# Performance work log

Measured on AMD Instinct MI355X. Metric: run time of the kernel, lower is better.

The kernel has to match this reference:

```python
import jax, jax.numpy as jnp
import numpy as np

NUM_LAYERS = 4
HID = 512
EMB = 512
VOCAB = 50000
SOU_LEN = 256
TAR_LEN = 50
BATCH = 8
VEXT = VOCAB + SOU_LEN


def _gru_layer(x, h0, wih, whh, bih, bhh):
    # x: [B,T,in], h0: [B,H]; PyTorch GRU gate order: r, z, n
    def step(h, xt):
        gi = xt @ wih.T + bih
        gh = h @ whh.T + bhh
        ir, iz, inn = jnp.split(gi, 3, axis=-1)
        hr, hz, hn = jnp.split(gh, 3, axis=-1)
        r = jax.nn.sigmoid(ir + hr)
        z = jax.nn.sigmoid(iz + hz)
        n = jnp.tanh(inn + r * hn)
        h_new = (1.0 - z) * n + z * h
        return h_new, h_new
    _, ys = jax.lax.scan(step, h0, jnp.swapaxes(x, 0, 1))
    return jnp.swapaxes(ys, 0, 1)


def _forward(sou, tar, hidden, encoder_outputs, extended_length,
             emb, gru_wih, gru_whh, gru_bih, gru_bhh,
             fc_enc_w, fc_enc_b, fc_dec_w, fc_dec_b, v_w,
             fc_out1_w, fc_out1_b, fc_out2_w, fc_out2_b,
             g1_w, g1_b, g2_w, g2_b, g3_w, g3_b):
    emb = emb.at[0].set(0.0)  # padding_idx=0 (also zeroes its grad)
    tar_emb = emb[tar]  # [B,T,E]
    # pack_padded_sequence: only first `length` steps processed, rest padded with 0
    lengths = jnp.maximum(jnp.sum(tar > 0, axis=-1), 1)
    x = tar_emb
    for l in range(gru_wih.shape[0]):
        x = _gru_layer(x, hidden[l], gru_wih[l], gru_whh[l], gru_bih[l], gru_bhh[l])
    t_idx = jnp.arange(x.shape[1])
    dec_out = jnp.where((t_idx[None, :] < lengths[:, None])[:, :, None], x, 0.0)  # [B,T,H]
    # additive (Bahdanau) attention
    e1 = encoder_outputs @ fc_enc_w.T + fc_enc_b          # [B,S,H]
    e2 = dec_out @ fc_dec_w.T + fc_dec_b                  # [B,T,H]
    energy = jnp.tanh(e1[:, None, :, :] + e2[:, :, None, :])  # [B,T,S,H]
    scores = jnp.einsum('btsh,h->bts', energy, v_w)
    scores = jnp.where((sou == 0)[:, None, :], -jnp.inf, scores)
    atten = jax.nn.softmax(scores, axis=-1)               # [B,T,S]
    weighted = jnp.einsum('bts,bsh->bth', atten, encoder_outputs)
    all_out = jnp.concatenate([weighted, dec_out], axis=-1)  # [B,T,2H]
    mid = all_out @ fc_out2_w.T + fc_out2_b
    logits = mid @ fc_out1_w.T + fc_out1_b                # [B,T,VEXT]
    # extended-vocab mask (vectorized version of the per-batch python loop)
    col = jnp.arange(logits.shape[-1])
    valid = col[None, None, :] < (VOCAB + extended_length)[:, None, None]
    logits = jnp.where(valid, logits, -1e9)
    output_gen = jax.nn.softmax(logits, axis=-1)
    # copy mechanism: scatter-add attention into extended vocab (replaces sparse one-hot bmm)
    def _scatter(att_b, sou_b):
        return jnp.zeros((att_b.shape[0], VEXT), att_b.dtype).at[:, sou_b].add(att_b)
    output_copy = jax.vmap(_scatter)(atten, sou)          # [B,T,VEXT]
    gate = jax.nn.sigmoid(
        jnp.einsum('bth,h->bt', weighted, g1_w) + g1_b[0]
        + jnp.einsum('bth,h->bt', dec_out, g2_w) + g2_b[0]
        + jnp.einsum('bte,e->bt', tar_emb, g3_w) + g3_b[0])[:, :, None]
    output = (1.0 - gate) * output_gen + gate * output_copy
    return output, atten


def setup_inputs() -> dict:
    key = jax.random.key(0)
    ks = jax.random.split(key, 24)
    s = 0.02
    return {
        'sou': jax.random.randint(ks[0], (BATCH, SOU_LEN), 0, VEXT),
        'tar': jax.random.randint(ks[1], (BATCH, TAR_LEN), 0, VEXT),
        'hidden': jax.random.normal(ks[2], (NUM_LAYERS, BATCH, HID), jnp.float32),
        'encoder_outputs': jax.random.normal(ks[3], (BATCH, SOU_LEN, HID), jnp.float32),
        'extended_length': jax.random.randint(ks[4], (BATCH,), 0, SOU_LEN),
        'emb': jax.random.normal(ks[5], (VEXT, EMB), jnp.float32) * s,
        'gru_wih': jax.random.normal(ks[6], (NUM_LAYERS, 3 * HID, EMB), jnp.float32) * s,
        'gru_whh': jax.random.normal(ks[7], (NUM_LAYERS, 3 * HID, HID), jnp.float32) * s,
        'gru_bih': jax.random.normal(ks[8], (NUM_LAYERS, 3 * HID), jnp.float32) * s,
        'gru_bhh': jax.random.normal(ks[9], (NUM_LAYERS, 3 * HID), jnp.float32) * s,
        'fc_enc_w': jax.random.normal(ks[10], (HID, HID), jnp.float32) * s,
        'fc_enc_b': jax.random.normal(ks[11], (HID,), jnp.float32) * s,
        'fc_dec_w': jax.random.normal(ks[12], (HID, HID), jnp.float32) * s,
        'fc_dec_b': jax.random.normal(ks[13], (HID,), jnp.float32) * s,
        'v_w': jax.random.normal(ks[14], (HID,), jnp.float32) * s,
        'fc_out1_w': jax.random.normal(ks[15], (VEXT, HID), jnp.float32) * s,
        'fc_out1_b': jax.random.normal(ks[16], (VEXT,), jnp.float32) * s,
        'fc_out2_w': jax.random.normal(ks[17], (HID, 2 * HID), jnp.float32) * s,
        'fc_out2_b': jax.random.normal(ks[18], (HID,), jnp.float32) * s,
        'g1_w': jax.random.normal(ks[19], (HID,), jnp.float32) * s,
        'g1_b': jnp.zeros((1,), jnp.float32),
        'g2_w': jax.random.normal(ks[20], (HID,), jnp.float32) * s,
        'g2_b': jnp.zeros((1,), jnp.float32),
        'g3_w': jax.random.normal(ks[21], (EMB,), jnp.float32) * s,
        'g3_b': jnp.zeros((1,), jnp.float32),
    }


def reference(sou, tar, hidden, encoder_outputs, extended_length,
              emb, gru_wih, gru_whh, gru_bih, gru_bhh,
              fc_enc_w, fc_enc_b, fc_dec_w, fc_dec_b, v_w,
              fc_out1_w, fc_out1_b, fc_out2_w, fc_out2_b,
              g1_w, g1_b, g2_w, g2_b, g3_w, g3_b):
    return _forward(sou, tar, hidden, encoder_outputs, extended_length,
                    emb, gru_wih, gru_whh, gru_bih, gru_bhh,
                    fc_enc_w, fc_enc_b, fc_dec_w, fc_dec_b, v_w,
                    fc_out1_w, fc_out1_b, fc_out2_w, fc_out2_b,
                    g1_w, g1_b, g2_w, g2_b, g3_w, g3_b)
```

## Files before the change

### kernel.cpp

```cpp
#include <hip/hip_runtime.h>

typedef unsigned short u16;
typedef unsigned int u32;
typedef unsigned long long u64;

using bf16x8 = __attribute__((ext_vector_type(8))) short;
using f32x4  = __attribute__((ext_vector_type(4))) float;

#define VOCAB 50000
#define VEXT  50256
#define OUT_AT_OFF 20102400L

__device__ __forceinline__ u16 f2b(float f) {
  u32 x = __float_as_uint(f);
  u32 r = (x + 0x7fffu + ((x >> 16) & 1u)) >> 16;
  return (u16)r;
}

__device__ __forceinline__ u32 sload32(const u32* p) {
  return __hip_atomic_load(p, __ATOMIC_RELAXED, __HIP_MEMORY_SCOPE_SYSTEM);
}
__device__ __forceinline__ u64 sload64(const u64* p) {
  return __hip_atomic_load(p, __ATOMIC_RELAXED, __HIP_MEMORY_SCOPE_SYSTEM);
}
__device__ __forceinline__ void sstore64(u64* p, u64 v) {
  __hip_atomic_store(p, v, __ATOMIC_RELAXED, __HIP_MEMORY_SCOPE_SYSTEM);
}
__device__ __forceinline__ bf16x8 sload8x(const u64* p) {
  union { u64 u[2]; bf16x8 v; } x;
  x.u[0] = sload64(p); x.u[1] = sload64(p + 1);
  return x.v;
}
__device__ __forceinline__ void wait_cnt(const u32* c, u32 target) {
  unsigned it = 0;
  while (sload32(c) < target) {
    __builtin_amdgcn_s_sleep(2);
    if (++it > (1u << 20)) break;
  }
  asm volatile("" ::: "memory");
}

__global__ void k_conv(const float* __restrict__ src, u16* __restrict__ dst,
                       long realN, long totalN) {
  long i = (long)blockIdx.x * 256 + threadIdx.x;
  if (i >= totalN) return;
  float v = (i < realN) ? src[i] : 0.f;
  dst[i] = f2b(v);
}

__global__ void k_h0b(const float* __restrict__ hidden, u16* __restrict__ h0B) {
  int i = blockIdx.x * 256 + threadIdx.x;
  int l = i >> 13, rem = i & 8191, rr = rem >> 9, k = rem & 511;
  float v = (rr < 8) ? hidden[((long)l * 8 + rr) * 512 + k] : 0.f;
  h0B[i] = f2b(v);
}

__global__ __launch_bounds__(256) void k_prep(const int* __restrict__ tar,
                                              const float* __restrict__ emb,
                                              const float* __restrict__ g3w,
                                              u16* __restrict__ xB0,
                                              float* __restrict__ g3dot) {
  int r = blockIdx.x;
  int tid = threadIdx.x;
  int idx = tar[r];
  __shared__ float red[256];
  float p = 0.f;
  for (int k = tid; k < 512; k += 256) {
    float v = (idx == 0) ? 0.f : emb[(long)idx * 512 + k];
    xB0[(long)r * 512 + k] = f2b(v);
    p += v * g3w[k];
  }
  red[tid] = p; __syncthreads();
  for (int o = 128; o > 0; o >>= 1) { if (tid < o) red[tid] += red[tid + o]; __syncthreads(); }
  if (tid == 0) g3dot[r] = red[0];
}

__global__ void k_lengths(const int* __restrict__ tar, int* __restrict__ lens) {
  int b = threadIdx.x;
  if (b < 8) {
    int c = 0;
    for (int t = 0; t < 50; t++) c += (tar[b * 50 + t] > 0) ? 1 : 0;
    lens[b] = (c > 0) ? c : 1;
  }
}

__global__ __launch_bounds__(256) void k_mask(float* __restrict__ x4f,
                                              const int* __restrict__ lens) {
  int r = blockIdx.x, b = r / 50, t = r % 50;
  if (t >= lens[b])
    for (int k = threadIdx.x; k < 512; k += 256) x4f[(long)r * 512 + k] = 0.f;
}

__global__ __launch_bounds__(128, 1) void k_gru(
    const u16* __restrict__ wihB, const u16* __restrict__ whhB,
    const float* __restrict__ bih, const float* __restrict__ bhh,
    const float* __restrict__ hidden, const u16* __restrict__ h0B,
    u16* __restrict__ xB,
    u32* __restrict__ hX,
    float* __restrict__ x4f,
    u32* __restrict__ cnt)
{
  const int wg = blockIdx.x;
  const int l = wg >> 5;
  const int c0 = (wg & 31) << 4;
  const int tid = threadIdx.x;
  const int wv = tid >> 6;
  const int lane = tid & 63;
  const int lrow = lane & 15;
  const int q = lane >> 4;

  __shared__ float giX[2][3][16][16];

  const u16* Wsrc = (wv == 0 ? wihB : whhB) + (long)l * 1536 * 512;

  const int col = c0 + lrow;
  const float bir = bih[l * 1536 + col],         bhr = bhh[l * 1536 + col];
  const float biz = bih[l * 1536 + 512 + col],   bhz = bhh[l * 1536 + 512 + col];
  const float bin_ = bih[l * 1536 + 1024 + col], bhn = bhh[l * 1536 + 1024 + col];

  const u16* xin = xB + (long)l * 16 * 50 * 512;

  float hreg[4];
  if (wv == 1) {
#pragma unroll
    for (int rg = 0; rg < 4; rg++) {
      int bb = q * 4 + rg;
      hreg[rg] = (bb < 8) ? hidden[((long)l * 8 + bb) * 512 + col] : 0.f;
    }
  }

  for (int t = 0; t < 50; t++) {
    bf16x8 af[16];
    if (wv == 0) {
      if (l > 0) {
        wait_cnt(cnt + (l - 1) * 16, 32u * (u32)(t + 1));
        const u64* A64 = (const u64*)((const u32*)xin + (long)lrow * 50 * 256 + (long)t * 256);
#pragma unroll
        for (int ks = 0; ks < 16; ks++) af[ks] = sload8x(A64 + ks * 8 + q * 2);
      } else {
        const u16* Asrc = xin + (long)lrow * 50 * 512 + (long)t * 512;
#pragma unroll
        for (int ks = 0; ks < 16; ks++) af[ks] = *(const bf16x8*)(Asrc + ks * 32 + q * 8);
      }
    } else {
      if (t > 0) {
        wait_cnt(cnt + l * 16, 32u * (u32)t);
        const u64* H64 = (const u64*)(hX + (((long)l * 2 + ((t - 1) & 1)) * 16 + lrow) * 256);
#pragma unroll
        for (int ks = 0; ks < 16; ks++) af[ks] = sload8x(H64 + ks * 8 + q * 2);
      } else {
        const u16* Asrc = h0B + ((long)l * 16 + lrow) * 512;
#pragma unroll
        for (int ks = 0; ks < 16; ks++) af[ks] = *(const bf16x8*)(Asrc + ks * 32 + q * 8);
      }
    }

    f32x4 a0 = {0.f, 0.f, 0.f, 0.f}, a1 = {0.f, 0.f, 0.f, 0.f}, a2 = {0.f, 0.f, 0.f, 0.f};
#pragma unroll
    for (int ks = 0; ks < 16; ks++) {
      bf16x8 b0 = *(const bf16x8*)(Wsrc + (long)(0 * 512 + c0 + lrow) * 512 + ks * 32 + q * 8);
      bf16x8 b1 = *(const bf16x8*)(Wsrc + (long)(1 * 512 + c0 + lrow) * 512 + ks * 32 + q * 8);
      bf16x8 b2 = *(const bf16x8*)(Wsrc + (long)(2 * 512 + c0 + lrow) * 512 + ks * 32 + q * 8);
      a0 = __builtin_amdgcn_mfma_f32_16x16x32_bf16(af[ks], b0, a0, 0, 0, 0);
      a1 = __builtin_amdgcn_mfma_f32_16x16x32_bf16(af[ks], b1, a1, 0, 0, 0);
      a2 = __builtin_amdgcn_mfma_f32_16x16x32_bf16(af[ks], b2, a2, 0, 0, 0);
    }

    if (wv == 0) {
#pragma unroll
      for (int rg = 0; rg < 4; rg++) {
        giX[t & 1][0][q * 4 + rg][lrow] = a0[rg];
        giX[t & 1][1][q * 4 + rg][lrow] = a1[rg];
        giX[t & 1][2][q * 4 + rg][lrow] = a2[rg];
      }
    }
    __syncthreads();

    if (wv == 1) {
#pragma unroll
      for (int rg = 0; rg < 4; rg++) {
        int bb = q * 4 + rg;
        float hnew = 0.f;
        u16 hb16 = 0;
        if (bb < 8) {
          float gir = giX[t & 1][0][bb][lrow] + bir;
          float giz = giX[t & 1][1][bb][lrow] + biz;
          float gin = giX[t & 1][2][bb][lrow] + bin_;
          float ghr = a0[rg] + bhr;
          float ghz = a1[rg] + bhz;
          float ghn = a2[rg] + bhn;
          float hprev = hreg[rg];
          float rr = 1.f / (1.f + expf(-(gir + ghr)));
          float zz = 1.f / (1.f + expf(-(giz + ghz)));
          float nn = tanhf(gin + rr * ghn);
          hnew = (1.f - zz) * nn + zz * hprev;
          hreg[rg] = hnew;
          hb16 = f2b(hnew);
        }
        u32 p32 = (u32)hb16 | ((u32)(u16)__shfl_xor((int)hb16, 1) << 16);
        u64 p64 = (u64)p32 | ((u64)(u32)__shfl_xor((int)p32, 2) << 32);
        if (bb < 8) {
          if ((lrow & 3) == 0) {
            long slot = ((long)l * 2 + (t & 1)) * 16 + bb;
            sstore64((u64*)hX + slot * 128 + (col >> 2), p64);
            if (l < 3)
              sstore64((u64*)xB + ((((long)(l + 1) * 16 + bb) * 50 + t) * 128) + (col >> 2), p64);
          }
          if (l == 3) x4f[((long)bb * 50 + t) * 512 + col] = hnew;
        }
      }
      asm volatile("s_waitcnt vmcnt(0)" ::: "memory");
      if (lane == 0)
        __hip_atomic_fetch_add(cnt + (long)l * 16, 1u,
                               __ATOMIC_RELAXED, __HIP_MEMORY_SCOPE_SYSTEM);
    }
  }
}

__global__ __launch_bounds__(256, 2) void k_gemm_bf16(
    const u16* __restrict__ A, const u16* __restrict__ Bm,
    const float* __restrict__ bias, float* __restrict__ C,
    int M, int N, int K, int ldc)
{
  __shared__ __align__(16) u16 As[4096];
  __shared__ __align__(16) u16 Bs[4096];
  const int tid = threadIdx.x;
  const int wv = tid >> 6, lane = tid & 63;
  const int wm = wv >> 1, wn = wv & 1;
  const int lrow = lane & 15, q = lane >> 4;
  const int m0 = blockIdx.y * 128, n0 = blockIdx.x * 128;

  f32x4 acc[4][4];
#pragma unroll
  for (int i = 0; i < 4; i++)
#pragma unroll
    for (int j = 0; j < 4; j++) acc[i][j] = {0.f, 0.f, 0.f, 0.f};

  for (int k0 = 0; k0 < K; k0 += 32) {
#pragma unroll
    for (int i = 0; i < 2; i++) {
      int c = i * 256 + tid;
      int row = c >> 2, ko = (c & 3) << 3;
      *(uint4*)(As + c * 8) = *(const uint4*)(A + (long)(m0 + row) * K + k0 + ko);
      *(uint4*)(Bs + c * 8) = *(const uint4*)(Bm + (long)(n0 + row) * K + k0 + ko);
    }
    __syncthreads();
    bf16x8 af[4], bfr[4];
#pragma unroll
    for (int i = 0; i < 4; i++) af[i] = *(const bf16x8*)(As + (wm * 64 + i * 16 + lrow) * 32 + q * 8);
#pragma unroll
    for (int j = 0; j < 4; j++) bfr[j] = *(const bf16x8*)(Bs + (wn * 64 + j * 16 + lrow) * 32 + q * 8);
#pragma unroll
    for (int i = 0; i < 4; i++)
#pragma unroll
      for (int j = 0; j < 4; j++)
        acc[i][j] = __builtin_amdgcn_mfma_f32_16x16x32_bf16(af[i], bfr[j], acc[i][j], 0, 0, 0);
    __syncthreads();
  }

#pragma unroll
  for (int i = 0; i < 4; i++) {
    int rbase = m0 + wm * 64 + i * 16 + q * 4;
#pragma unroll
    for (int j = 0; j < 4; j++) {
      int colg = n0 + wn * 64 + j * 16 + lrow;
      if (colg < N) {
        float bv = bias[colg];
#pragma unroll
        for (int rg = 0; rg < 4; rg++) {
          int rowg = rbase + rg;
          if (rowg < M) C[(long)rowg * ldc + colg] = acc[i][j][rg] + bv;
        }
      }
    }
  }
}

__global__ __launch_bounds__(256) void k_attn(
    const float* __restrict__ e1, const float* __restrict__ e2,
    const float* __restrict__ enc, const float* __restrict__ x4f,
    const int* __restrict__ sou, const float* __restrict__ vw,
    const float* __restrict__ g1w, const float* __restrict__ g1b,
    const float* __restrict__ g2w, const float* __restrict__ g2b,
    const float* __restrict__ g3b, const float* __restrict__ g3dot,
    float* __restrict__ all_out, float* __restrict__ gate,
    float* __restrict__ atten_out)
{
  int r = blockIdx.x;
  int b = r / 50;
  int tid = threadIdx.x;
  __shared__ float e2s[512], decs[512], at[256], red[256];
  for (int k = tid; k < 512; k += 256) {
    e2s[k] = e2[(long)r * 512 + k];
    decs[k] = x4f[(long)r * 512 + k];
  }
  __syncthreads();
  const float* erow = e1 + ((long)b * 256 + tid) * 512;
  float sc = 0.f;
#pragma unroll 4
  for (int h = 0; h < 512; h++) sc += vw[h] * tanhf(erow[h] + e2s[h]);
  if (sou[b * 256 + tid] == 0) sc = -INFINITY;

  red[tid] = sc; __syncthreads();
  for (int o = 128; o > 0; o >>= 1) { if (tid < o) red[tid] = fmaxf(red[tid], red[tid + o]); __syncthreads(); }
  float mx = red[0]; __syncthreads();
  float p = expf(sc - mx);
  red[tid] = p; __syncthreads();
  for (int o = 128; o > 0; o >>= 1) { if (tid < o) red[tid] += red[tid + o]; __syncthreads(); }
  float S = red[0]; __syncthreads();
  float a = p / S;
  at[tid] = a;
  atten_out[(long)r * 256 + tid] = a;
  __syncthreads();

  float pg = 0.f;
  for (int h = tid; h < 512; h += 256) {
    float wsum = 0.f;
    const float* ecol = enc + (long)b * 256 * 512 + h;
    for (int s = 0; s < 256; s++) wsum += at[s] * ecol[(long)s * 512];
    all_out[(long)r * 1024 + h] = wsum;
    all_out[(long)r * 1024 + 512 + h] = decs[h];
    pg += wsum * g1w[h] + decs[h] * g2w[h];
  }
  red[tid] = pg; __syncthreads();
  for (int o = 128; o > 0; o >>= 1) { if (tid < o) red[tid] += red[tid + o]; __syncthreads(); }
  if (tid == 0) {
    float z = red[0] + g1b[0] + g2b[0] + g3dot[r] + g3b[0];
    gate[r] = 1.f / (1.f + expf(-z));
  }
}

__global__ __launch_bounds__(1024) void k_softmax(float* __restrict__ out,
                                                  const float* __restrict__ gate,
                                                  const int* __restrict__ ext) {
  int r = blockIdx.x;
  int b = r / 50;
  int tid = threadIdx.x;
  int nv = VOCAB + ext[b];
  __shared__ float red[1024];
  float* row = out + (long)r * VEXT;
  float m = -INFINITY;
  for (int c = tid; c < nv; c += 1024) m = fmaxf(m, row[c]);
  red[tid] = m; __syncthreads();
  for (int o = 512; o > 0; o >>= 1) { if (tid < o) red[tid] = fmaxf(red[tid], red[tid + o]); __syncthreads(); }
  m = red[0]; __syncthreads();
  float s = 0.f;
  for (int c = tid; c < nv; c += 1024) s += expf(row[c] - m);
  red[tid] = s; __syncthreads();
  for (int o = 512; o > 0; o >>= 1) { if (tid < o) red[tid] += red[tid + o]; __syncthreads(); }
  float inv = (1.f - gate[r]) / red[0];
  for (int c = tid; c < VEXT; c += 1024) {
    float v = (c < nv) ? expf(row[c] - m) * inv : 0.f;
    row[c] = v;
  }
}

__global__ void k_scatter(float* __restrict__ out, const float* __restrict__ atten,
                          const float* __restrict__ gate, const int* __restrict__ sou) {
  int r = blockIdx.x, s = threadIdx.x;
  int b = r / 50;
  float v = gate[r] * atten[(long)r * 256 + s];
  int colv = sou[b * 256 + s];
  atomicAdd(out + (long)r * VEXT + colv, v);
}

extern "C" void kernel_launch(void* const* d_in, const int* in_sizes, int n_in,
                              void* d_out, int out_size, void* d_ws, size_t ws_size,
                              hipStream_t stream) {
  (void)in_sizes; (void)n_in; (void)out_size;
  const int* sou = (const int*)d_in[0];
  const int* tar = (const int*)d_in[1];
  const float* hidden = (const float*)d_in[2];
  const float* enc = (const float*)d_in[3];
  const int* ext = (const int*)d_in[4];
  const float* emb = (const float*)d_in[5];
  const float* wih = (const float*)d_in[6];
  const float* whh = (const float*)d_in[7];
  const float* bih = (const float*)d_in[8];
  const float* bhh = (const float*)d_in[9];
  const float* fc_enc_w = (const float*)d_in[10];
  const float* fc_enc_b = (const float*)d_in[11];
  const float* fc_dec_w = (const float*)d_in[12];
  const float* fc_dec_b = (const float*)d_in[13];
  const float* v_w = (const float*)d_in[14];
  const float* w1 = (const float*)d_in[15];
  const float* b1 = (const float*)d_in[16];
  const float* w2 = (const float*)d_in[17];
  const float* b2 = (const float*)d_in[18];
  const float* g1w = (const float*)d_in[19];
  const float* g1b = (const float*)d_in[20];
  const float* g2w = (const float*)d_in[21];
  const float* g2b = (const float*)d_in[22];
  const float* g3w = (const float*)d_in[23];
  const float* g3b = (const float*)d_in[24];
  float* out = (float*)d_out;

  char* base = (char*)d_ws;
  size_t cur = 0;
  auto alloc = [&](size_t bytes) -> void* {
    void* r = base + cur;
    cur = (cur + bytes + 255) & ~(size_t)255;
    return r;
  };
  u16* wihB = (u16*)alloc(6291456);
  u16* whhB = (u16*)alloc(6291456);
  u16* w1B  = (u16*)alloc(51511296);
  u16* encB = (u16*)alloc(2097152);
  u16* fceB = (u16*)alloc(524288);
  u16* fcdB = (u16*)alloc(524288);
  u16* fo2B = (u16*)alloc(1048576);
  u16* midB = (u16*)alloc(524288);
  u16* decB = (u16*)alloc(524288);
  u16* allB = (u16*)alloc(1048576);
  u16* xB   = (u16*)alloc(3276800);
  u16* h0B  = (u16*)alloc(65536);
  u32* hX   = (u32*)alloc(131072);
  float* x4f = (float*)alloc(819200);
  float* e1 = (float*)alloc(4194304);
  float* e2 = (float*)alloc(819200);
  float* allo = (float*)alloc(1638400);
  float* mid = (float*)alloc(819200);
  float* g3dot = (float*)alloc(1600);
  float* gate = (float*)alloc(1600);
  int* lens = (int*)alloc(32);
  u32* cnt = (u32*)alloc(256);
  if (cur > ws_size) return;

  hipMemsetAsync(cnt, 0, 256, stream);

  k_conv<<<12288, 256, 0, stream>>>(wih, wihB, 3145728L, 3145728L);
  k_conv<<<12288, 256, 0, stream>>>(whh, whhB, 3145728L, 3145728L);
  k_conv<<<100608, 256, 0, stream>>>(w1, w1B, 25731072L, 25755648L);
  k_conv<<<4096, 256, 0, stream>>>(enc, encB, 1048576L, 1048576L);
  k_conv<<<1024, 256, 0, stream>>>(fc_enc_w, fceB, 262144L, 262144L);
  k_conv<<<1024, 256, 0, stream>>>(fc_dec_w, fcdB, 262144L, 262144L);
  k_conv<<<2048, 256, 0, stream>>>(w2, fo2B, 524288L, 524288L);
  k_h0b<<<128, 256, 0, stream>>>(hidden, h0B);
  k_prep<<<400, 256, 0, stream>>>(tar, emb, g3w, xB, g3dot);
  k_lengths<<<1, 64, 0, stream>>>(tar, lens);

  k_gru<<<128, 128, 0, stream>>>(wihB, whhB, bih, bhh, hidden, h0B, xB, hX, x4f, cnt);
  k_mask<<<400, 256, 0, stream>>>(x4f, lens);
  k_conv<<<1024, 256, 0, stream>>>(x4f, decB, 204800L, 262144L);

  k_gemm_bf16<<<dim3(4, 16), 256, 0, stream>>>(encB, fceB, fc_enc_b, e1, 2048, 512, 512, 512);
  k_gemm_bf16<<<dim3(4, 4), 256, 0, stream>>>(decB, fcdB, fc_dec_b, e2, 400, 512, 512, 512);
  k_attn<<<400, 256, 0, stream>>>(e1, e2, enc, x4f, sou, v_w, g1w, g1b, g2w, g2b, g3b,
                                  g3dot, allo, gate, out + OUT_AT_OFF);
  k_conv<<<2048, 256, 0, stream>>>(allo, allB, 409600L, 524288L);
  k_gemm_bf16<<<dim3(4, 4), 256, 0, stream>>>(allB, fo2B, b2, mid, 400, 512, 1024, 512);
  k_conv<<<1024, 256, 0, stream>>>(mid, midB, 204800L, 262144L);

  k_gemm_bf16<<<dim3(393, 4), 256, 0, stream>>>(midB, w1B, b1, out, 400, 50256, 512, 50256);
  k_softmax<<<400, 1024, 0, stream>>>(out, gate, ext);
  k_scatter<<<400, 256, 0, stream>>>(out, out + OUT_AT_OFF, gate, sou);
}
```

Measured before the change: 1.107 ms.

## Overlap w1 bf16 conversion with GRU, split counters, restructure attention and softmax

Moves the large fc_out1 weight fp32-to-bf16 conversion into 128 extra blocks of the latency-bound GRU kernel, so it runs on otherwise idle CUs during the recurrence. Replaces the single per-layer sync counter with four sub-counters polled in parallel to reduce atomic contention. Rewrites attention scoring so each wave reduces over h with coalesced loads, and makes the weighted sum coalesced. Fuses the softmax max and sum passes into an online softmax and folds the scatter kernel into it. The risk is that co-resident conversion blocks compete for bandwidth or CU slots with the GRU blocks, which depend on spin-waiting.

```diff
diff --git a/kernel.cpp b/kernel.cpp
--- a/kernel.cpp
+++ b/kernel.cpp
@@ -31,9 +31,12 @@
   x.u[0] = sload64(p); x.u[1] = sload64(p + 1);
   return x.v;
 }
-__device__ __forceinline__ void wait_cnt(const u32* c, u32 target) {
+__device__ __forceinline__ void wait_cnt4(const u32* c4, u32 tgt) {
+  const u32* p = c4 + (threadIdx.x & 3) * 16;
   unsigned it = 0;
-  while (sload32(c) < target) {
+  while (true) {
+    u32 v = sload32(p);
+    if (__all((int)(v >= tgt))) break;
     __builtin_amdgcn_s_sleep(2);
     if (++it > (1u << 20)) break;
   }
@@ -98,12 +101,30 @@
     u16* __restrict__ xB,
     u32* __restrict__ hX,
     float* __restrict__ x4f,
-    u32* __restrict__ cnt)
+    u32* __restrict__ cnt,
+    const float* __restrict__ w1src, u16* __restrict__ w1B)
 {
   const int wg = blockIdx.x;
+  const int tid = threadIdx.x;
+
+  if (wg >= 128) {
+    long tidg = (long)(wg - 128) * 128 + tid;
+    const float4* src4 = (const float4*)w1src;
+#pragma unroll 4
+    for (int it = 0; it < 393; it++) {
+      long e = tidg * 4 + (long)it * 65536;
+      float4 v = {0.f, 0.f, 0.f, 0.f};
+      if (e < 25731072L) v = src4[e >> 2];
+      u64 o = (u64)f2b(v.x) | ((u64)f2b(v.y) << 16) |
+              ((u64)f2b(v.z) << 32) | ((u64)f2b(v.w) << 48);
+      *(u64*)(w1B + e) = o;
+    }
+    return;
+  }
+
   const int l = wg >> 5;
-  const int c0 = (wg & 31) << 4;
-  const int tid = threadIdx.x;
+  const int wg32 = wg & 31;
+  const int c0 = wg32 << 4;
   const int wv = tid >> 6;
   const int lane = tid & 63;
   const int lrow = lane & 15;
@@ -133,7 +154,7 @@
     bf16x8 af[16];
     if (wv == 0) {
       if (l > 0) {
-        wait_cnt(cnt + (l - 1) * 16, 32u * (u32)(t + 1));
+        wait_cnt4(cnt + (l - 1) * 64, 8u * (u32)(t + 1));
         const u64* A64 = (const u64*)((const u32*)xin + (long)lrow * 50 * 256 + (long)t * 256);
 #pragma unroll
         for (int ks = 0; ks < 16; ks++) af[ks] = sload8x(A64 + ks * 8 + q * 2);
@@ -144,7 +165,7 @@
       }
     } else {
       if (t > 0) {
-        wait_cnt(cnt + l * 16, 32u * (u32)t);
+        wait_cnt4(cnt + l * 64, 8u * (u32)t);
         const u64* H64 = (const u64*)(hX + (((long)l * 2 + ((t - 1) & 1)) * 16 + lrow) * 256);
 #pragma unroll
         for (int ks = 0; ks < 16; ks++) af[ks] = sload8x(H64 + ks * 8 + q * 2);
@@ -211,7 +232,7 @@
       }
       asm volatile("s_waitcnt vmcnt(0)" ::: "memory");
       if (lane == 0)
-        __hip_atomic_fetch_add(cnt + (long)l * 16, 1u,
+        __hip_atomic_fetch_add(cnt + (long)l * 64 + (wg32 >> 3) * 16, 1u,
                                __ATOMIC_RELAXED, __HIP_MEMORY_SCOPE_SYSTEM);
     }
   }
@@ -289,18 +310,30 @@
   int r = blockIdx.x;
   int b = r / 50;
   int tid = threadIdx.x;
+  int wv = tid >> 6, lane = tid & 63;
   __shared__ float e2s[512], decs[512], at[256], red[256];
   for (int k = tid; k < 512; k += 256) {
     e2s[k] = e2[(long)r * 512 + k];
     decs[k] = x4f[(long)r * 512 + k];
   }
   __syncthreads();
-  const float* erow = e1 + ((long)b * 256 + tid) * 512;
-  float sc = 0.f;
-#pragma unroll 4
-  for (int h = 0; h < 512; h++) sc += vw[h] * tanhf(erow[h] + e2s[h]);
+
+  for (int s = wv; s < 256; s += 4) {
+    const float* row = e1 + ((long)b * 256 + s) * 512;
+    float acc = 0.f;
+#pragma unroll
+    for (int c = 0; c < 8; c++) {
+      int h = c * 64 + lane;
+      acc += vw[h] * tanhf(row[h] + e2s[h]);
+    }
+#pragma unroll
+    for (int o = 32; o > 0; o >>= 1) acc += __shfl_xor(acc, o);
+    if (lane == 0) at[s] = acc;
+  }
+  __syncthreads();
+
+  float sc = at[tid];
   if (sou[b * 256 + tid] == 0) sc = -INFINITY;
-
   red[tid] = sc; __syncthreads();
   for (int o = 128; o > 0; o >>= 1) { if (tid < o) red[tid] = fmaxf(red[tid], red[tid + o]); __syncthreads(); }
   float mx = red[0]; __syncthreads();
@@ -313,15 +346,19 @@
   atten_out[(long)r * 256 + tid] = a;
   __syncthreads();
 
-  float pg = 0.f;
-  for (int h = tid; h < 512; h += 256) {
-    float wsum = 0.f;
-    const float* ecol = enc + (long)b * 256 * 512 + h;
-    for (int s = 0; s < 256; s++) wsum += at[s] * ecol[(long)s * 512];
-    all_out[(long)r * 1024 + h] = wsum;
-    all_out[(long)r * 1024 + 512 + h] = decs[h];
-    pg += wsum * g1w[h] + decs[h] * g2w[h];
-  }
+  float acc0 = 0.f, acc1 = 0.f;
+  const float* eb = enc + (long)b * 256 * 512;
+  for (int s = 0; s < 256; s++) {
+    float a_s = at[s];
+    acc0 += a_s * eb[(long)s * 512 + tid];
+    acc1 += a_s * eb[(long)s * 512 + tid + 256];
+  }
+  all_out[(long)r * 1024 + tid] = acc0;
+  all_out[(long)r * 1024 + tid + 256] = acc1;
+  all_out[(long)r * 1024 + 512 + tid] = decs[tid];
+  all_out[(long)r * 1024 + 512 + tid + 256] = decs[tid + 256];
+  float pg = acc0 * g1w[tid] + acc1 * g1w[tid + 256]
+           + decs[tid] * g2w[tid] + decs[tid + 256] * g2w[tid + 256];
   red[tid] = pg; __syncthreads();
   for (int o = 128; o > 0; o >>= 1) { if (tid < o) red[tid] += red[tid + o]; __syncthreads(); }
   if (tid == 0) {
@@ -332,36 +369,43 @@
 
 __global__ __launch_bounds__(1024) void k_softmax(float* __restrict__ out,
                                                   const float* __restrict__ gate,
-                                                  const int* __restrict__ ext) {
+                                                  const int* __restrict__ ext,
+                                                  const float* __restrict__ atten,
+                                                  const int* __restrict__ sou) {
   int r = blockIdx.x;
   int b = r / 50;
   int tid = threadIdx.x;
   int nv = VOCAB + ext[b];
-  __shared__ float red[1024];
+  __shared__ float redm[1024];
+  __shared__ float reds[1024];
   float* row = out + (long)r * VEXT;
-  float m = -INFINITY;
-  for (int c = tid; c < nv; c += 1024) m = fmaxf(m, row[c]);
-  red[tid] = m; __syncthreads();
-  for (int o = 512; o > 0; o >>= 1) { if (tid < o) red[tid] = fmaxf(red[tid], red[tid + o]); __syncthreads(); }
-  m = red[0]; __syncthreads();
-  float s = 0.f;
-  for (int c = tid; c < nv; c += 1024) s += expf(row[c] - m);
-  red[tid] = s; __syncthreads();
-  for (int o = 512; o > 0; o >>= 1) { if (tid < o) red[tid] += red[tid + o]; __syncthreads(); }
-  float inv = (1.f - gate[r]) / red[0];
+  float m = -INFINITY, s = 0.f;
+  for (int c = tid; c < nv; c += 1024) {
+    float v = row[c];
+    if (v > m) { s = s * expf(m - v) + 1.f; m = v; }
+    else s += expf(v - m);
+  }
+  redm[tid] = m; reds[tid] = s; __syncthreads();
+  for (int o = 512; o > 0; o >>= 1) {
+    if (tid < o) {
+      float m1 = redm[tid], s1 = reds[tid], m2 = redm[tid + o], s2 = reds[tid + o];
+      float M = fmaxf(m1, m2);
+      redm[tid] = M;
+      reds[tid] = s1 * expf(m1 - M) + s2 * expf(m2 - M);
+    }
+    __syncthreads();
+  }
+  float M = redm[0];
+  float inv = (1.f - gate[r]) / reds[0];
   for (int c = tid; c < VEXT; c += 1024) {
-    float v = (c < nv) ? expf(row[c] - m) * inv : 0.f;
+    float v = (c < nv) ? expf(row[c] - M) * inv : 0.f;
     row[c] = v;
   }
-}
-
-__global__ void k_scatter(float* __restrict__ out, const float* __restrict__ atten,
-                          const float* __restrict__ gate, const int* __restrict__ sou) {
-  int r = blockIdx.x, s = threadIdx.x;
-  int b = r / 50;
-  float v = gate[r] * atten[(long)r * 256 + s];
-  int colv = sou[b * 256 + s];
-  atomicAdd(out + (long)r * VEXT + colv, v);
+  __syncthreads();
+  if (tid < 256) {
+    float v = gate[r] * atten[(long)r * 256 + tid];
+    atomicAdd(row + sou[b * 256 + tid], v);
+  }
 }
 
 extern "C" void kernel_launch(void* const* d_in, const int* in_sizes, int n_in,
@@ -423,14 +467,13 @@
   float* g3dot = (float*)alloc(1600);
   float* gate = (float*)alloc(1600);
   int* lens = (int*)alloc(32);
-  u32* cnt = (u32*)alloc(256);
+  u32* cnt = (u32*)alloc(1024);
   if (cur > ws_size) return;
 
-  hipMemsetAsync(cnt, 0, 256, stream);
+  hipMemsetAsync(cnt, 0, 1024, stream);
 
   k_conv<<<12288, 256, 0, stream>>>(wih, wihB, 3145728L, 3145728L);
   k_conv<<<12288, 256, 0, stream>>>(whh, whhB, 3145728L, 3145728L);
-  k_conv<<<100608, 256, 0, stream>>>(w1, w1B, 25731072L, 25755648L);
   k_conv<<<4096, 256, 0, stream>>>(enc, encB, 1048576L, 1048576L);
   k_conv<<<1024, 256, 0, stream>>>(fc_enc_w, fceB, 262144L, 262144L);
   k_conv<<<1024, 256, 0, stream>>>(fc_dec_w, fcdB, 262144L, 262144L);
@@ -439,7 +482,8 @@
   k_prep<<<400, 256, 0, stream>>>(tar, emb, g3w, xB, g3dot);
   k_lengths<<<1, 64, 0, stream>>>(tar, lens);
 
-  k_gru<<<128, 128, 0, stream>>>(wihB, whhB, bih, bhh, hidden, h0B, xB, hX, x4f, cnt);
+  k_gru<<<256, 128, 0, stream>>>(wihB, whhB, bih, bhh, hidden, h0B, xB, hX, x4f, cnt,
+                                 w1, w1B);
   k_mask<<<400, 256, 0, stream>>>(x4f, lens);
   k_conv<<<1024, 256, 0, stream>>>(x4f, decB, 204800L, 262144L);
 
@@ -452,6 +496,5 @@
   k_conv<<<1024, 256, 0, stream>>>(mid, midB, 204800L, 262144L);
 
   k_gemm_bf16<<<dim3(393, 4), 256, 0, stream>>>(midB, w1B, b1, out, 400, 50256, 512, 50256);
-  k_softmax<<<400, 1024, 0, stream>>>(out, gate, ext);
-  k_scatter<<<400, 256, 0, stream>>>(out, out + OUT_AT_OFF, gate, sou);
-}
+  k_softmax<<<400, 1024, 0, stream>>>(out, gate, ext, out + OUT_AT_OFF, sou);
+}
```

After: 1.038 ms. 6.2% less time.
